# Kernel tuning notes

Measured on AMD Instinct MI355X. Metric: run time of the kernel, lower is better.

## Reference

```python
import jax, jax.numpy as jnp
import numpy as np

B, E, F_IN = 8192, 64, 7
D, H = 64, 4           # feature_size, heads
HD = D // H            # features per head


def setup_inputs() -> dict:
    key = jax.random.key(0)
    ks = jax.random.split(key, 14)
    def lin(k, i, o):
        return jax.random.normal(k, (i, o), jnp.float32) * (1.0 / np.sqrt(i))
    return {
        "x": jax.random.normal(ks[0], (B, E, F_IN), jnp.float32),
        # ego embedding MLP (7->64->64, with bias)
        "ego_w0": lin(ks[1], F_IN, D), "ego_b0": jnp.zeros((D,), jnp.float32),
        "ego_w1": lin(ks[2], D, D),    "ego_b1": jnp.zeros((D,), jnp.float32),
        # others embedding MLP (separate weights)
        "oth_w0": lin(ks[3], F_IN, D), "oth_b0": jnp.zeros((D,), jnp.float32),
        "oth_w1": lin(ks[4], D, D),    "oth_b1": jnp.zeros((D,), jnp.float32),
        # attention projections (no bias)
        "Wk": lin(ks[5], D, D), "Wv": lin(ks[6], D, D),
        "Wq": lin(ks[7], D, D), "Wc": lin(ks[8], D, D),
    }


def _mlp(x, w0, b0, w1, b1):
    h = jax.nn.relu(x @ w0 + b0)
    return jax.nn.relu(h @ w1 + b1)


def reference(x, ego_w0, ego_b0, ego_w1, ego_b1,
              oth_w0, oth_b0, oth_w1, oth_b1, Wk, Wv, Wq, Wc):
    b = x.shape[0]
    mask = x[:, :, 0] < 0.5                       # [B, E] absent entities
    ego = _mlp(x[:, 0:1, :], ego_w0, ego_b0, ego_w1, ego_b1)   # [B, 1, D]
    others = _mlp(x[:, 1:, :], oth_w0, oth_b0, oth_w1, oth_b1)  # [B, E-1, D]
    input_all = jnp.concatenate([ego, others], axis=1)          # [B, E, D]

    # project and split heads -> [B, H, E, HD]
    k = (input_all @ Wk).reshape(b, E, H, HD).transpose(0, 2, 1, 3)
    v = (input_all @ Wv).reshape(b, E, H, HD).transpose(0, 2, 1, 3)
    q = (ego @ Wq).reshape(b, 1, H, HD).transpose(0, 2, 1, 3)   # [B, H, 1, HD]

    scores = jnp.einsum('bhqd,bhkd->bhqk', q, k) / np.sqrt(HD)  # [B, H, 1, E]
    scores = jnp.where(mask[:, None, None, :], -1e9, scores)
    p_attn = jax.nn.softmax(scores, axis=-1)
    out = jnp.einsum('bhqk,bhkd->bhqd', p_attn, v)              # [B, H, 1, HD]
    out = out.reshape(b, D)                                      # concat heads
    result = (out @ Wc + ego[:, 0, :]) * 0.5                     # [B, D]
    return result
```

## Files before the change

### kernel.cpp

```cpp
#include <hip/hip_runtime.h>
#include <hip/hip_bf16.h>


typedef __attribute__((ext_vector_type(8))) short short8;
typedef __attribute__((ext_vector_type(4))) short short4b;
typedef __attribute__((ext_vector_type(4))) float f32x4;

#define SY 72

__device__ __forceinline__ short f2bs(float x) {
    __hip_bfloat16 h = __float2bfloat16(x);
    return __builtin_bit_cast(short, h);
}
__device__ __forceinline__ float bs2f(short s) {
    __hip_bfloat16 h = __builtin_bit_cast(__hip_bfloat16, s);
    return __bfloat162float(h);
}

__global__ void transpose_wk(const float* __restrict__ Wk, float* __restrict__ WkT) {
    const int c = blockIdx.x;
    const int g = threadIdx.x;
    WkT[c * 64 + g] = Wk[g * 64 + c];
}

__global__ __launch_bounds__(64, 2)
void ego_attn_kernel(const float* __restrict__ x,
                     const float* __restrict__ ego_w0, const float* __restrict__ ego_b0,
                     const float* __restrict__ ego_w1, const float* __restrict__ ego_b1,
                     const float* __restrict__ oth_w0, const float* __restrict__ oth_b0,
                     const float* __restrict__ oth_w1, const float* __restrict__ oth_b1,
                     const float* __restrict__ Wk, const float* __restrict__ WkT,
                     const float* __restrict__ Wv,
                     const float* __restrict__ Wq, const float* __restrict__ Wc,
                     float* __restrict__ out, int use_wkt)
{
    __shared__ __align__(16) short hy[64 * SY];
    __shared__ __align__(16) short kqt[16 * SY];
    __shared__ __align__(16) short pa[16 * SY];
    __shared__ __align__(16) float mb[64];
    __shared__ __align__(16) short pyb[4 * 68];
    __shared__ __align__(16) float ob[64];

    const int lane = threadIdx.x;
    const int lg = lane >> 4, ln = lane & 15;
    const int b = blockIdx.x;
    const float* xb = x + (size_t)b * 448;

    mb[lane] = xb[lane * 7];

    float x0[7] = {0, 0, 0, 0, 0, 0, 0};
    short8 xa[4];
#pragma unroll
    for (int mt = 0; mt < 4; ++mt) {
        short8 v = {0, 0, 0, 0, 0, 0, 0, 0};
        if (lg == 0) {
            const float* xr = xb + (mt * 16 + ln) * 7;
            float t[7];
#pragma unroll
            for (int i = 0; i < 7; ++i) t[i] = xr[i];
            if (mt == 0) {
#pragma unroll
                for (int i = 0; i < 7; ++i) x0[i] = t[i];
            }
#pragma unroll
            for (int i = 0; i < 7; ++i) v[i] = f2bs(t[i]);
        }
        xa[mt] = v;
    }

    short8 w0f[4];
#pragma unroll
    for (int ct = 0; ct < 4; ++ct) {
        short8 v = {0, 0, 0, 0, 0, 0, 0, 0};
        if (lg == 0) {
#pragma unroll
            for (int j = 0; j < 7; ++j) v[j] = f2bs(oth_w0[j * 64 + ct * 16 + ln]);
        }
        w0f[ct] = v;
    }
    short8 w1f[2][4];
#pragma unroll
    for (int kc = 0; kc < 2; ++kc)
#pragma unroll
        for (int ct = 0; ct < 4; ++ct) {
            short8 v;
#pragma unroll
            for (int j = 0; j < 8; ++j)
                v[j] = f2bs(oth_w1[(kc * 32 + lg * 8 + j) * 64 + ct * 16 + ln]);
            w1f[kc][ct] = v;
        }
    float b0v[4], b1v[4];
#pragma unroll
    for (int ct = 0; ct < 4; ++ct) {
        b0v[ct] = oth_b0[ct * 16 + ln];
        b1v[ct] = oth_b1[ct * 16 + ln];
    }
    const float b0e = ego_b0[lane], b1e = ego_b1[lane];
    float w0e[7];
#pragma unroll
    for (int i = 0; i < 7; ++i) w0e[i] = ego_w0[i * 64 + lane];

    float acc = b0e;
#pragma unroll
    for (int i = 0; i < 7; ++i) acc = fmaf(__shfl(x0[i], 0), w0e[i], acc);
    const float hego = fmaxf(acc, 0.f);

#pragma unroll
    for (int mt = 0; mt < 4; ++mt)
#pragma unroll
        for (int ct = 0; ct < 4; ++ct) {
            f32x4 c = {b0v[ct], b0v[ct], b0v[ct], b0v[ct]};
            c = __builtin_amdgcn_mfma_f32_16x16x32_bf16(xa[mt], w0f[ct], c, 0, 0, 0);
#pragma unroll
            for (int r = 0; r < 4; ++r)
                hy[(mt * 16 + lg * 4 + r) * SY + ct * 16 + ln] = f2bs(fmaxf(c[r], 0.f));
        }
    __syncthreads();

    short8 a2[4][2];
#pragma unroll
    for (int mt = 0; mt < 4; ++mt)
#pragma unroll
        for (int kc = 0; kc < 2; ++kc)
            a2[mt][kc] = *(const short8*)&hy[(mt * 16 + ln) * SY + kc * 32 + lg * 8];
    __syncthreads();

    acc = b1e;
#pragma unroll
    for (int j = 0; j < 64; ++j)
        acc = fmaf(__shfl(hego, j), ego_w1[j * 64 + lane], acc);
    const float ego = fmaxf(acc, 0.f);

#pragma unroll
    for (int ct = 0; ct < 4; ++ct)
#pragma unroll
        for (int mt = 0; mt < 4; ++mt) {
            f32x4 c = {b1v[ct], b1v[ct], b1v[ct], b1v[ct]};
            c = __builtin_amdgcn_mfma_f32_16x16x32_bf16(a2[mt][0], w1f[0][ct], c, 0, 0, 0);
            c = __builtin_amdgcn_mfma_f32_16x16x32_bf16(a2[mt][1], w1f[1][ct], c, 0, 0, 0);
#pragma unroll
            for (int r = 0; r < 4; ++r)
                hy[(mt * 16 + lg * 4 + r) * SY + ct * 16 + ln] = f2bs(fmaxf(c[r], 0.f));
        }
    hy[lane] = f2bs(ego);

    float qf = 0.f;
#pragma unroll
    for (int j = 0; j < 64; ++j)
        qf = fmaf(__shfl(ego, j), Wq[j * 64 + lane], qf);
    float kqh[4] = {0.f, 0.f, 0.f, 0.f};
    if (use_wkt) {
#pragma unroll
        for (int j = 0; j < 64; ++j) {
            const float qj = __shfl(qf, j);
            kqh[j >> 4] = fmaf(WkT[j * 64 + lane], qj, kqh[j >> 4]);
        }
    } else {
#pragma unroll
        for (int j = 0; j < 64; ++j) {
            const float qj = __shfl(qf, j);
            kqh[j >> 4] = fmaf(Wk[lane * 64 + j], qj, kqh[j >> 4]);
        }
    }
#pragma unroll
    for (int h = 0; h < 4; ++h) kqt[h * SY + lane] = f2bs(kqh[h]);
    __syncthreads();

    short8 ya[4][2];
#pragma unroll
    for (int mt = 0; mt < 4; ++mt)
#pragma unroll
        for (int kc = 0; kc < 2; ++kc)
            ya[mt][kc] = *(const short8*)&hy[(mt * 16 + ln) * SY + kc * 32 + lg * 8];
    short8 kb[2];
#pragma unroll
    for (int kc = 0; kc < 2; ++kc)
        kb[kc] = *(const short8*)&kqt[ln * SY + kc * 32 + lg * 8];

    float sv[16];
    float m = -3e38f;
#pragma unroll
    for (int mt = 0; mt < 4; ++mt) {
        f32x4 c = {0.f, 0.f, 0.f, 0.f};
        c = __builtin_amdgcn_mfma_f32_16x16x32_bf16(ya[mt][0], kb[0], c, 0, 0, 0);
        c = __builtin_amdgcn_mfma_f32_16x16x32_bf16(ya[mt][1], kb[1], c, 0, 0, 0);
        const float4 mk = *(const float4*)&mb[mt * 16 + lg * 4];
        const float mkv[4] = {mk.x, mk.y, mk.z, mk.w};
#pragma unroll
        for (int r = 0; r < 4; ++r) {
            float s = c[r] * 0.25f;
            if (mkv[r] < 0.5f) s = -1e9f;
            sv[mt * 4 + r] = s;
            m = fmaxf(m, s);
        }
    }
    m = fmaxf(m, __shfl_xor(m, 16));
    m = fmaxf(m, __shfl_xor(m, 32));
    float sum = 0.f;
#pragma unroll
    for (int k = 0; k < 16; ++k) { sv[k] = __expf(sv[k] - m); sum += sv[k]; }
    sum += __shfl_xor(sum, 16);
    sum += __shfl_xor(sum, 32);
    const float inv = 1.f / sum;
#pragma unroll
    for (int mt = 0; mt < 4; ++mt) {
        short4b pk;
#pragma unroll
        for (int r = 0; r < 4; ++r) pk[r] = f2bs(sv[mt * 4 + r] * inv);
        *(short4b*)&pa[ln * SY + mt * 16 + lg * 4] = pk;
    }
    __syncthreads();

    short8 pf[2];
#pragma unroll
    for (int kc = 0; kc < 2; ++kc)
        pf[kc] = *(const short8*)&pa[ln * SY + kc * 32 + lg * 8];
#pragma unroll
    for (int ct = 0; ct < 4; ++ct) {
        f32x4 c = {0.f, 0.f, 0.f, 0.f};
#pragma unroll
        for (int kc = 0; kc < 2; ++kc) {
            short8 yv;
#pragma unroll
            for (int j = 0; j < 8; ++j)
                yv[j] = hy[(kc * 32 + lg * 8 + j) * SY + ct * 16 + ln];
            c = __builtin_amdgcn_mfma_f32_16x16x32_bf16(pf[kc], yv, c, 0, 0, 0);
        }
        if (lg == 0) {
#pragma unroll
            for (int r = 0; r < 4; ++r) pyb[r * 68 + ct * 16 + ln] = f2bs(c[r]);
        }
    }
    __syncthreads();

    const int h = lane >> 4;
    float o = 0.f;
#pragma unroll
    for (int f4 = 0; f4 < 16; ++f4) {
        const short4b pv = *(const short4b*)&pyb[h * 68 + f4 * 4];
#pragma unroll
        for (int u = 0; u < 4; ++u)
            o = fmaf(bs2f(pv[u]), Wv[(f4 * 4 + u) * 64 + lane], o);
    }
    ob[lane] = o;
    __syncthreads();

    float r2 = 0.f;
#pragma unroll
    for (int j4 = 0; j4 < 16; ++j4) {
        const float4 ov = *(const float4*)&ob[j4 * 4];
        const float ovv[4] = {ov.x, ov.y, ov.z, ov.w};
#pragma unroll
        for (int u = 0; u < 4; ++u)
            r2 = fmaf(ovv[u], Wc[(j4 * 4 + u) * 64 + lane], r2);
    }
    out[(size_t)b * 64 + lane] = (r2 + ego) * 0.5f;
}

extern "C" void kernel_launch(void* const* d_in, const int* in_sizes, int n_in,
                              void* d_out, int out_size, void* d_ws, size_t ws_size,
                              hipStream_t stream) {
    const float* x      = (const float*)d_in[0];
    const float* ego_w0 = (const float*)d_in[1];
    const float* ego_b0 = (const float*)d_in[2];
    const float* ego_w1 = (const float*)d_in[3];
    const float* ego_b1 = (const float*)d_in[4];
    const float* oth_w0 = (const float*)d_in[5];
    const float* oth_b0 = (const float*)d_in[6];
    const float* oth_w1 = (const float*)d_in[7];
    const float* oth_b1 = (const float*)d_in[8];
    const float* Wk     = (const float*)d_in[9];
    const float* Wv     = (const float*)d_in[10];
    const float* Wq     = (const float*)d_in[11];
    const float* Wc     = (const float*)d_in[12];

    float* WkT = (float*)d_ws;
    const int use_wkt = (ws_size >= 64 * 64 * sizeof(float)) ? 1 : 0;
    if (use_wkt) transpose_wk<<<64, 64, 0, stream>>>(Wk, WkT);

    ego_attn_kernel<<<8192, 64, 0, stream>>>(
        x, ego_w0, ego_b0, ego_w1, ego_b1,
        oth_w0, oth_b0, oth_w1, oth_b1,
        Wk, WkT, Wv, Wq, Wc,
        (float*)d_out, use_wkt);
}
```

Baseline: 134.5 us.

## Batch four samples per block, fold Wq·Wk into packed bf16 weights

```diff
diff --git a/kernel.cpp b/kernel.cpp
--- a/kernel.cpp
+++ b/kernel.cpp
@@ -8,253 +8,314 @@
 
 #define SY 72
 
+#define WS_G    0
+#define WS_EGW0 16384
+#define WS_EGW1 16896
+#define WS_WVT  20992
+#define WS_WCT  25088
+#define WS_W0T  29184
+#define WS_W1T  29696
+
 __device__ __forceinline__ short f2bs(float x) {
     __hip_bfloat16 h = __float2bfloat16(x);
     return __builtin_bit_cast(short, h);
 }
-__device__ __forceinline__ float bs2f(short s) {
-    __hip_bfloat16 h = __builtin_bit_cast(__hip_bfloat16, s);
-    return __bfloat162float(h);
-}
-
-__global__ void transpose_wk(const float* __restrict__ Wk, float* __restrict__ WkT) {
-    const int c = blockIdx.x;
-    const int g = threadIdx.x;
-    WkT[c * 64 + g] = Wk[g * 64 + c];
+__device__ __forceinline__ unsigned short f2u(float x) {
+    __hip_bfloat16 h = __float2bfloat16(x);
+    return __builtin_bit_cast(unsigned short, h);
+}
+__device__ __forceinline__ short8 ldws8(const unsigned short* p) {
+    return *(const short8*)p;
+}
+
+__global__ void pack_ws(const float* __restrict__ ego_w0, const float* __restrict__ ego_w1,
+                        const float* __restrict__ oth_w0, const float* __restrict__ oth_w1,
+                        const float* __restrict__ Wk, const float* __restrict__ Wv,
+                        const float* __restrict__ Wq, const float* __restrict__ Wc,
+                        unsigned short* __restrict__ ws) {
+    const int blk = blockIdx.x, t = threadIdx.x;
+    if (blk < 256) {
+        const int n = blk, h = n >> 6, f = n & 63, j = t;
+        float a = 0.f;
+#pragma unroll
+        for (int d = 0; d < 16; ++d)
+            a = fmaf(Wq[j * 64 + h * 16 + d], Wk[f * 64 + h * 16 + d], a);
+        ws[WS_G + n * 64 + j] = f2u(a);
+    } else {
+        const int n = blk - 256, k = t;
+        ws[WS_EGW1 + n * 64 + k] = f2u(ego_w1[k * 64 + n]);
+        ws[WS_WVT  + n * 64 + k] = f2u(Wv[k * 64 + n]);
+        ws[WS_WCT  + n * 64 + k] = f2u(Wc[k * 64 + n]);
+        ws[WS_W1T  + n * 64 + k] = f2u(oth_w1[k * 64 + n]);
+        if (k < 8) {
+            ws[WS_EGW0 + n * 8 + k] = (k < 7) ? f2u(ego_w0[k * 64 + n]) : 0;
+            ws[WS_W0T  + n * 8 + k] = (k < 7) ? f2u(oth_w0[k * 64 + n]) : 0;
+        }
+    }
 }
 
 __global__ __launch_bounds__(64, 2)
 void ego_attn_kernel(const float* __restrict__ x,
-                     const float* __restrict__ ego_w0, const float* __restrict__ ego_b0,
-                     const float* __restrict__ ego_w1, const float* __restrict__ ego_b1,
-                     const float* __restrict__ oth_w0, const float* __restrict__ oth_b0,
-                     const float* __restrict__ oth_w1, const float* __restrict__ oth_b1,
-                     const float* __restrict__ Wk, const float* __restrict__ WkT,
-                     const float* __restrict__ Wv,
-                     const float* __restrict__ Wq, const float* __restrict__ Wc,
-                     float* __restrict__ out, int use_wkt)
+                     const float* __restrict__ ego_b0, const float* __restrict__ ego_b1,
+                     const float* __restrict__ oth_b0, const float* __restrict__ oth_b1,
+                     const unsigned short* __restrict__ ws,
+                     float* __restrict__ out)
 {
     __shared__ __align__(16) short hy[64 * SY];
-    __shared__ __align__(16) short kqt[16 * SY];
+    __shared__ __align__(16) short chainbuf[4 * SY];
+    __shared__ __align__(16) short kqb[16 * SY];
     __shared__ __align__(16) short pa[16 * SY];
+    __shared__ __align__(16) short py[16 * SY];
+    __shared__ __align__(16) short ob[4 * SY];
     __shared__ __align__(16) float mb[64];
-    __shared__ __align__(16) short pyb[4 * 68];
-    __shared__ __align__(16) float ob[64];
 
     const int lane = threadIdx.x;
     const int lg = lane >> 4, ln = lane & 15;
-    const int b = blockIdx.x;
-    const float* xb = x + (size_t)b * 448;
-
-    mb[lane] = xb[lane * 7];
-
-    float x0[7] = {0, 0, 0, 0, 0, 0, 0};
-    short8 xa[4];
-#pragma unroll
-    for (int mt = 0; mt < 4; ++mt) {
-        short8 v = {0, 0, 0, 0, 0, 0, 0, 0};
-        if (lg == 0) {
-            const float* xr = xb + (mt * 16 + ln) * 7;
-            float t[7];
-#pragma unroll
-            for (int i = 0; i < 7; ++i) t[i] = xr[i];
-            if (mt == 0) {
-#pragma unroll
-                for (int i = 0; i < 7; ++i) x0[i] = t[i];
-            }
-#pragma unroll
-            for (int i = 0; i < 7; ++i) v[i] = f2bs(t[i]);
-        }
-        xa[mt] = v;
-    }
-
-    short8 w0f[4];
-#pragma unroll
-    for (int ct = 0; ct < 4; ++ct) {
-        short8 v = {0, 0, 0, 0, 0, 0, 0, 0};
-        if (lg == 0) {
-#pragma unroll
-            for (int j = 0; j < 7; ++j) v[j] = f2bs(oth_w0[j * 64 + ct * 16 + ln]);
-        }
-        w0f[ct] = v;
-    }
-    short8 w1f[2][4];
+    const int gb = blockIdx.x * 4;
+
+    short8 w0f[4], w1f[2][4];
+#pragma unroll
+    for (int ct = 0; ct < 4; ++ct) {
+        short8 z = {0, 0, 0, 0, 0, 0, 0, 0};
+        w0f[ct] = (lg == 0) ? ldws8(ws + WS_W0T + (ct * 16 + ln) * 8) : z;
+    }
 #pragma unroll
     for (int kc = 0; kc < 2; ++kc)
 #pragma unroll
+        for (int ct = 0; ct < 4; ++ct)
+            w1f[kc][ct] = ldws8(ws + WS_W1T + (ct * 16 + ln) * 64 + kc * 32 + lg * 8);
+    float b0v[4], b1v[4], eb0v[4], eb1v[4];
+#pragma unroll
+    for (int ct = 0; ct < 4; ++ct) {
+        b0v[ct]  = oth_b0[ct * 16 + ln];
+        b1v[ct]  = oth_b1[ct * 16 + ln];
+        eb0v[ct] = ego_b0[ct * 16 + ln];
+        eb1v[ct] = ego_b1[ct * 16 + ln];
+    }
+
+    short8 xea = {0, 0, 0, 0, 0, 0, 0, 0};
+    if (lg == 0 && ln < 4) {
+        const float* xr = x + (size_t)(gb + ln) * 448;
+#pragma unroll
+        for (int i = 0; i < 7; ++i) xea[i] = f2bs(xr[i]);
+    }
+#pragma unroll
+    for (int ct = 0; ct < 4; ++ct) {
+        short8 z = {0, 0, 0, 0, 0, 0, 0, 0};
+        const short8 bfr = (lg == 0) ? ldws8(ws + WS_EGW0 + (ct * 16 + ln) * 8) : z;
+        f32x4 c = {eb0v[ct], eb0v[ct], eb0v[ct], eb0v[ct]};
+        c = __builtin_amdgcn_mfma_f32_16x16x32_bf16(xea, bfr, c, 0, 0, 0);
+        if (lg == 0) {
+#pragma unroll
+            for (int r = 0; r < 4; ++r)
+                chainbuf[r * SY + ct * 16 + ln] = f2bs(fmaxf(c[r], 0.f));
+        }
+    }
+    __syncthreads();
+    short8 ha[2];
+#pragma unroll
+    for (int kc = 0; kc < 2; ++kc)
+        ha[kc] = *(const short8*)&chainbuf[(ln & 3) * SY + kc * 32 + lg * 8];
+    __syncthreads();
+
+    float egoR[4][4];
+#pragma unroll
+    for (int ct = 0; ct < 4; ++ct) {
+        f32x4 c = {eb1v[ct], eb1v[ct], eb1v[ct], eb1v[ct]};
+#pragma unroll
+        for (int kc = 0; kc < 2; ++kc) {
+            const short8 bfr = ldws8(ws + WS_EGW1 + (ct * 16 + ln) * 64 + kc * 32 + lg * 8);
+            c = __builtin_amdgcn_mfma_f32_16x16x32_bf16(ha[kc], bfr, c, 0, 0, 0);
+        }
+#pragma unroll
+        for (int r = 0; r < 4; ++r) egoR[ct][r] = fmaxf(c[r], 0.f);
+    }
+    if (lg == 0) {
+#pragma unroll
+        for (int ct = 0; ct < 4; ++ct)
+#pragma unroll
+            for (int r = 0; r < 4; ++r)
+                chainbuf[r * SY + ct * 16 + ln] = f2bs(egoR[ct][r]);
+    }
+    __syncthreads();
+    short8 ea[2];
+#pragma unroll
+    for (int kc = 0; kc < 2; ++kc)
+        ea[kc] = *(const short8*)&chainbuf[(ln & 3) * SY + kc * 32 + lg * 8];
+
+#pragma unroll
+    for (int ctg = 0; ctg < 16; ++ctg) {
+        f32x4 c = {0.f, 0.f, 0.f, 0.f};
+#pragma unroll
+        for (int kc = 0; kc < 2; ++kc) {
+            const short8 bfr = ldws8(ws + WS_G + (ctg * 16 + ln) * 64 + kc * 32 + lg * 8);
+            c = __builtin_amdgcn_mfma_f32_16x16x32_bf16(ea[kc], bfr, c, 0, 0, 0);
+        }
+        if (lg == 0) {
+            const int h = ctg >> 2, fc = (ctg & 3) * 16 + ln;
+#pragma unroll
+            for (int r = 0; r < 4; ++r)
+                kqb[(r * 4 + h) * SY + fc] = f2bs(c[r] * 0.25f);
+        }
+    }
+    __syncthreads();
+
+#pragma unroll
+    for (int i = 0; i < 4; ++i) {
+        const float* xb = x + (size_t)(gb + i) * 448;
+        mb[lane] = xb[lane * 7];
+
+        short8 xa[4];
+#pragma unroll
+        for (int mt = 0; mt < 4; ++mt) {
+            short8 v = {0, 0, 0, 0, 0, 0, 0, 0};
+            if (lg == 0) {
+                const float* xr = xb + (mt * 16 + ln) * 7;
+#pragma unroll
+                for (int k = 0; k < 7; ++k) v[k] = f2bs(xr[k]);
+            }
+            xa[mt] = v;
+        }
+#pragma unroll
+        for (int mt = 0; mt < 4; ++mt)
+#pragma unroll
+            for (int ct = 0; ct < 4; ++ct) {
+                f32x4 c = {b0v[ct], b0v[ct], b0v[ct], b0v[ct]};
+                c = __builtin_amdgcn_mfma_f32_16x16x32_bf16(xa[mt], w0f[ct], c, 0, 0, 0);
+#pragma unroll
+                for (int r = 0; r < 4; ++r)
+                    hy[(mt * 16 + lg * 4 + r) * SY + ct * 16 + ln] = f2bs(fmaxf(c[r], 0.f));
+            }
+        __syncthreads();
+        short8 a2[4][2];
+#pragma unroll
+        for (int mt = 0; mt < 4; ++mt)
+#pragma unroll
+            for (int kc = 0; kc < 2; ++kc)
+                a2[mt][kc] = *(const short8*)&hy[(mt * 16 + ln) * SY + kc * 32 + lg * 8];
+        __syncthreads();
+#pragma unroll
+        for (int ct = 0; ct < 4; ++ct)
+#pragma unroll
+            for (int mt = 0; mt < 4; ++mt) {
+                f32x4 c = {b1v[ct], b1v[ct], b1v[ct], b1v[ct]};
+                c = __builtin_amdgcn_mfma_f32_16x16x32_bf16(a2[mt][0], w1f[0][ct], c, 0, 0, 0);
+                c = __builtin_amdgcn_mfma_f32_16x16x32_bf16(a2[mt][1], w1f[1][ct], c, 0, 0, 0);
+#pragma unroll
+                for (int r = 0; r < 4; ++r)
+                    hy[(mt * 16 + lg * 4 + r) * SY + ct * 16 + ln] = f2bs(fmaxf(c[r], 0.f));
+            }
+        if (lg == 0) {
+#pragma unroll
+            for (int ct = 0; ct < 4; ++ct)
+                hy[ct * 16 + ln] = f2bs(egoR[ct][i]);
+        }
+        __syncthreads();
+        short8 ya[4][2];
+#pragma unroll
+        for (int mt = 0; mt < 4; ++mt)
+#pragma unroll
+            for (int kc = 0; kc < 2; ++kc)
+                ya[mt][kc] = *(const short8*)&hy[(mt * 16 + ln) * SY + kc * 32 + lg * 8];
+        short8 kb[2];
+#pragma unroll
+        for (int kc = 0; kc < 2; ++kc)
+            kb[kc] = *(const short8*)&kqb[(i * 4 + (ln & 3)) * SY + kc * 32 + lg * 8];
+
+        float sv[16];
+        float m = -3e38f;
+#pragma unroll
+        for (int mt = 0; mt < 4; ++mt) {
+            f32x4 c = {0.f, 0.f, 0.f, 0.f};
+            c = __builtin_amdgcn_mfma_f32_16x16x32_bf16(ya[mt][0], kb[0], c, 0, 0, 0);
+            c = __builtin_amdgcn_mfma_f32_16x16x32_bf16(ya[mt][1], kb[1], c, 0, 0, 0);
+            const float4 mk = *(const float4*)&mb[mt * 16 + lg * 4];
+            const float mkv[4] = {mk.x, mk.y, mk.z, mk.w};
+#pragma unroll
+            for (int r = 0; r < 4; ++r) {
+                float s = c[r];
+                if (mkv[r] < 0.5f) s = -1e9f;
+                sv[mt * 4 + r] = s;
+                m = fmaxf(m, s);
+            }
+        }
+        m = fmaxf(m, __shfl_xor(m, 16));
+        m = fmaxf(m, __shfl_xor(m, 32));
+        float sum = 0.f;
+#pragma unroll
+        for (int k = 0; k < 16; ++k) { sv[k] = __expf(sv[k] - m); sum += sv[k]; }
+        sum += __shfl_xor(sum, 16);
+        sum += __shfl_xor(sum, 32);
+        const float inv = 1.f / sum;
+#pragma unroll
+        for (int mt = 0; mt < 4; ++mt) {
+            short4b pk;
+#pragma unroll
+            for (int r = 0; r < 4; ++r) pk[r] = f2bs(sv[mt * 4 + r] * inv);
+            *(short4b*)&pa[ln * SY + mt * 16 + lg * 4] = pk;
+        }
+        __syncthreads();
+        short8 pf[2];
+#pragma unroll
+        for (int kc = 0; kc < 2; ++kc)
+            pf[kc] = *(const short8*)&pa[ln * SY + kc * 32 + lg * 8];
+#pragma unroll
         for (int ct = 0; ct < 4; ++ct) {
-            short8 v;
-#pragma unroll
-            for (int j = 0; j < 8; ++j)
-                v[j] = f2bs(oth_w1[(kc * 32 + lg * 8 + j) * 64 + ct * 16 + ln]);
-            w1f[kc][ct] = v;
-        }
-    float b0v[4], b1v[4];
-#pragma unroll
-    for (int ct = 0; ct < 4; ++ct) {
-        b0v[ct] = oth_b0[ct * 16 + ln];
-        b1v[ct] = oth_b1[ct * 16 + ln];
-    }
-    const float b0e = ego_b0[lane], b1e = ego_b1[lane];
-    float w0e[7];
-#pragma unroll
-    for (int i = 0; i < 7; ++i) w0e[i] = ego_w0[i * 64 + lane];
-
-    float acc = b0e;
-#pragma unroll
-    for (int i = 0; i < 7; ++i) acc = fmaf(__shfl(x0[i], 0), w0e[i], acc);
-    const float hego = fmaxf(acc, 0.f);
-
-#pragma unroll
-    for (int mt = 0; mt < 4; ++mt)
-#pragma unroll
-        for (int ct = 0; ct < 4; ++ct) {
-            f32x4 c = {b0v[ct], b0v[ct], b0v[ct], b0v[ct]};
-            c = __builtin_amdgcn_mfma_f32_16x16x32_bf16(xa[mt], w0f[ct], c, 0, 0, 0);
-#pragma unroll
-            for (int r = 0; r < 4; ++r)
-                hy[(mt * 16 + lg * 4 + r) * SY + ct * 16 + ln] = f2bs(fmaxf(c[r], 0.f));
-        }
-    __syncthreads();
-
-    short8 a2[4][2];
-#pragma unroll
-    for (int mt = 0; mt < 4; ++mt)
+            f32x4 c = {0.f, 0.f, 0.f, 0.f};
+#pragma unroll
+            for (int kc = 0; kc < 2; ++kc) {
+                short8 yv;
+#pragma unroll
+                for (int j = 0; j < 8; ++j)
+                    yv[j] = hy[(kc * 32 + lg * 8 + j) * SY + ct * 16 + ln];
+                c = __builtin_amdgcn_mfma_f32_16x16x32_bf16(pf[kc], yv, c, 0, 0, 0);
+            }
+            if (lg == 0) {
+#pragma unroll
+                for (int r = 0; r < 4; ++r)
+                    py[(r * 4 + i) * SY + ct * 16 + ln] = f2bs(c[r]);
+            }
+        }
+        __syncthreads();
+    }
+
+#pragma unroll
+    for (int ct = 0; ct < 4; ++ct) {
+        short8 af[2];
 #pragma unroll
         for (int kc = 0; kc < 2; ++kc)
-            a2[mt][kc] = *(const short8*)&hy[(mt * 16 + ln) * SY + kc * 32 + lg * 8];
-    __syncthreads();
-
-    acc = b1e;
-#pragma unroll
-    for (int j = 0; j < 64; ++j)
-        acc = fmaf(__shfl(hego, j), ego_w1[j * 64 + lane], acc);
-    const float ego = fmaxf(acc, 0.f);
-
-#pragma unroll
-    for (int ct = 0; ct < 4; ++ct)
-#pragma unroll
-        for (int mt = 0; mt < 4; ++mt) {
-            f32x4 c = {b1v[ct], b1v[ct], b1v[ct], b1v[ct]};
-            c = __builtin_amdgcn_mfma_f32_16x16x32_bf16(a2[mt][0], w1f[0][ct], c, 0, 0, 0);
-            c = __builtin_amdgcn_mfma_f32_16x16x32_bf16(a2[mt][1], w1f[1][ct], c, 0, 0, 0);
-#pragma unroll
-            for (int r = 0; r < 4; ++r)
-                hy[(mt * 16 + lg * 4 + r) * SY + ct * 16 + ln] = f2bs(fmaxf(c[r], 0.f));
-        }
-    hy[lane] = f2bs(ego);
-
-    float qf = 0.f;
-#pragma unroll
-    for (int j = 0; j < 64; ++j)
-        qf = fmaf(__shfl(ego, j), Wq[j * 64 + lane], qf);
-    float kqh[4] = {0.f, 0.f, 0.f, 0.f};
-    if (use_wkt) {
-#pragma unroll
-        for (int j = 0; j < 64; ++j) {
-            const float qj = __shfl(qf, j);
-            kqh[j >> 4] = fmaf(WkT[j * 64 + lane], qj, kqh[j >> 4]);
-        }
-    } else {
-#pragma unroll
-        for (int j = 0; j < 64; ++j) {
-            const float qj = __shfl(qf, j);
-            kqh[j >> 4] = fmaf(Wk[lane * 64 + j], qj, kqh[j >> 4]);
-        }
-    }
-#pragma unroll
-    for (int h = 0; h < 4; ++h) kqt[h * SY + lane] = f2bs(kqh[h]);
-    __syncthreads();
-
-    short8 ya[4][2];
-#pragma unroll
-    for (int mt = 0; mt < 4; ++mt)
-#pragma unroll
-        for (int kc = 0; kc < 2; ++kc)
-            ya[mt][kc] = *(const short8*)&hy[(mt * 16 + ln) * SY + kc * 32 + lg * 8];
-    short8 kb[2];
+            af[kc] = *(const short8*)&py[(ct * 4 + (ln & 3)) * SY + kc * 32 + lg * 8];
+        f32x4 c = {0.f, 0.f, 0.f, 0.f};
+#pragma unroll
+        for (int kc = 0; kc < 2; ++kc) {
+            const short8 bfr = ldws8(ws + WS_WVT + (ct * 16 + ln) * 64 + kc * 32 + lg * 8);
+            c = __builtin_amdgcn_mfma_f32_16x16x32_bf16(af[kc], bfr, c, 0, 0, 0);
+        }
+        if (lg == 0) {
+#pragma unroll
+            for (int r = 0; r < 4; ++r)
+                ob[r * SY + ct * 16 + ln] = f2bs(c[r]);
+        }
+    }
+    __syncthreads();
+    short8 oa[2];
 #pragma unroll
     for (int kc = 0; kc < 2; ++kc)
-        kb[kc] = *(const short8*)&kqt[ln * SY + kc * 32 + lg * 8];
-
-    float sv[16];
-    float m = -3e38f;
-#pragma unroll
-    for (int mt = 0; mt < 4; ++mt) {
+        oa[kc] = *(const short8*)&ob[(ln & 3) * SY + kc * 32 + lg * 8];
+#pragma unroll
+    for (int ct = 0; ct < 4; ++ct) {
         f32x4 c = {0.f, 0.f, 0.f, 0.f};
-        c = __builtin_amdgcn_mfma_f32_16x16x32_bf16(ya[mt][0], kb[0], c, 0, 0, 0);
-        c = __builtin_amdgcn_mfma_f32_16x16x32_bf16(ya[mt][1], kb[1], c, 0, 0, 0);
-        const float4 mk = *(const float4*)&mb[mt * 16 + lg * 4];
-        const float mkv[4] = {mk.x, mk.y, mk.z, mk.w};
-#pragma unroll
-        for (int r = 0; r < 4; ++r) {
-            float s = c[r] * 0.25f;
-            if (mkv[r] < 0.5f) s = -1e9f;
-            sv[mt * 4 + r] = s;
-            m = fmaxf(m, s);
-        }
-    }
-    m = fmaxf(m, __shfl_xor(m, 16));
-    m = fmaxf(m, __shfl_xor(m, 32));
-    float sum = 0.f;
-#pragma unroll
-    for (int k = 0; k < 16; ++k) { sv[k] = __expf(sv[k] - m); sum += sv[k]; }
-    sum += __shfl_xor(sum, 16);
-    sum += __shfl_xor(sum, 32);
-    const float inv = 1.f / sum;
-#pragma unroll
-    for (int mt = 0; mt < 4; ++mt) {
-        short4b pk;
-#pragma unroll
-        for (int r = 0; r < 4; ++r) pk[r] = f2bs(sv[mt * 4 + r] * inv);
-        *(short4b*)&pa[ln * SY + mt * 16 + lg * 4] = pk;
-    }
-    __syncthreads();
-
-    short8 pf[2];
-#pragma unroll
-    for (int kc = 0; kc < 2; ++kc)
-        pf[kc] = *(const short8*)&pa[ln * SY + kc * 32 + lg * 8];
-#pragma unroll
-    for (int ct = 0; ct < 4; ++ct) {
-        f32x4 c = {0.f, 0.f, 0.f, 0.f};
 #pragma unroll
         for (int kc = 0; kc < 2; ++kc) {
-            short8 yv;
-#pragma unroll
-            for (int j = 0; j < 8; ++j)
-                yv[j] = hy[(kc * 32 + lg * 8 + j) * SY + ct * 16 + ln];
-            c = __builtin_amdgcn_mfma_f32_16x16x32_bf16(pf[kc], yv, c, 0, 0, 0);
-        }
-        if (lg == 0) {
-#pragma unroll
-            for (int r = 0; r < 4; ++r) pyb[r * 68 + ct * 16 + ln] = f2bs(c[r]);
-        }
-    }
-    __syncthreads();
-
-    const int h = lane >> 4;
-    float o = 0.f;
-#pragma unroll
-    for (int f4 = 0; f4 < 16; ++f4) {
-        const short4b pv = *(const short4b*)&pyb[h * 68 + f4 * 4];
-#pragma unroll
-        for (int u = 0; u < 4; ++u)
-            o = fmaf(bs2f(pv[u]), Wv[(f4 * 4 + u) * 64 + lane], o);
-    }
-    ob[lane] = o;
-    __syncthreads();
-
-    float r2 = 0.f;
-#pragma unroll
-    for (int j4 = 0; j4 < 16; ++j4) {
-        const float4 ov = *(const float4*)&ob[j4 * 4];
-        const float ovv[4] = {ov.x, ov.y, ov.z, ov.w};
-#pragma unroll
-        for (int u = 0; u < 4; ++u)
-            r2 = fmaf(ovv[u], Wc[(j4 * 4 + u) * 64 + lane], r2);
-    }
-    out[(size_t)b * 64 + lane] = (r2 + ego) * 0.5f;
+            const short8 bfr = ldws8(ws + WS_WCT + (ct * 16 + ln) * 64 + kc * 32 + lg * 8);
+            c = __builtin_amdgcn_mfma_f32_16x16x32_bf16(oa[kc], bfr, c, 0, 0, 0);
+        }
+        if (lg == 0) {
+#pragma unroll
+            for (int r = 0; r < 4; ++r)
+                out[(size_t)(gb + r) * 64 + ct * 16 + ln] = (c[r] + egoR[ct][r]) * 0.5f;
+        }
+    }
 }
 
 extern "C" void kernel_launch(void* const* d_in, const int* in_sizes, int n_in,
@@ -274,13 +335,9 @@
     const float* Wq     = (const float*)d_in[11];
     const float* Wc     = (const float*)d_in[12];
 
-    float* WkT = (float*)d_ws;
-    const int use_wkt = (ws_size >= 64 * 64 * sizeof(float)) ? 1 : 0;
-    if (use_wkt) transpose_wk<<<64, 64, 0, stream>>>(Wk, WkT);
-
-    ego_attn_kernel<<<8192, 64, 0, stream>>>(
-        x, ego_w0, ego_b0, ego_w1, ego_b1,
-        oth_w0, oth_b0, oth_w1, oth_b1,
-        Wk, WkT, Wv, Wq, Wc,
-        (float*)d_out, use_wkt);
-}
+    unsigned short* ws = (unsigned short*)d_ws;
+    pack_ws<<<320, 64, 0, stream>>>(ego_w0, ego_w1, oth_w0, oth_w1,
+                                    Wk, Wv, Wq, Wc, ws);
+    ego_attn_kernel<<<2048, 64, 0, stream>>>(
+        x, ego_b0, ego_b1, oth_b0, oth_b1, ws, (float*)d_out);
+}
```

Measured after the change: 122.0 us. 1.1x faster.
